# Optimization experiments

Measured on AMD Instinct MI355X. Metric: run time of the kernel, lower is better.

## Reference

```python
import jax, jax.numpy as jnp
import numpy as np
import math

D = 1024
H = 16
EPS = 1e-5

def _layernorm(x, gamma, beta):
    mu = jnp.mean(x, axis=-1, keepdims=True)
    var = jnp.var(x, axis=-1, keepdims=True)
    return (x - mu) * jax.lax.rsqrt(var + EPS) * gamma + beta

def setup_inputs() -> dict:
    key = jax.random.key(0)
    ks = jax.random.split(key, 6)
    B, T = 2, 2048
    x = jax.random.normal(ks[0], (B, T, D), dtype=jnp.float32)
    s = 1.0 / math.sqrt(D)
    Wq = jax.random.normal(ks[1], (D, D), dtype=jnp.float32) * s
    Wk = jax.random.normal(ks[2], (D, D), dtype=jnp.float32) * s
    Wv = jax.random.normal(ks[3], (D, D), dtype=jnp.float32) * s
    gamma = jnp.ones((D,), dtype=jnp.float32)
    beta = jnp.zeros((D,), dtype=jnp.float32)
    return {"x": x, "Wq": Wq, "Wk": Wk, "Wv": Wv, "gamma": gamma, "beta": beta}

def reference(x, Wq, Wk, Wv, gamma, beta):
    B, T, Dm = x.shape
    hd = Dm // H
    xn = _layernorm(x, gamma, beta)
    # torch Linear (no bias): y = x @ W.T
    q = (xn @ Wq.T).reshape(B, T, H, hd)
    k = (xn @ Wk.T).reshape(B, T, H, hd)
    v = (xn @ Wv.T).reshape(B, T, H, hd)
    scale = 1.0 / math.sqrt(hd)
    att = jnp.einsum('bnhd,bmhd->bnmh', q, k) * scale  # B,T,T,H
    w = jax.nn.softmax(att, axis=2)  # softmax over key dim m
    y = jnp.einsum('bnmh,bmhd->bnhd', w, v).reshape(B, T, Dm)
    return x + y
```

## Files before the change

### kernel.cpp

```cpp
#include <hip/hip_runtime.h>
#include <hip/hip_bf16.h>
#include <stdint.h>

#define D_MODEL 1024
#define T_SEQ   2048
#define NB      2
#define NH      16
#define HD      64
#define MTOK    4096

typedef __bf16  bf16x8 __attribute__((ext_vector_type(8)));
typedef float   f32x4  __attribute__((ext_vector_type(4)));
typedef float   f32x16 __attribute__((ext_vector_type(16)));

#define GPTR(p) ((const __attribute__((address_space(1))) void*)(p))
#define LPTR(p) ((__attribute__((address_space(3))) void*)(p))

static __device__ __forceinline__ ushort f2bf(float f) {
    union { float f; uint32_t u; } c{f};
    uint32_t u = c.u;
    return (ushort)((u + 0x7fff + ((u >> 16) & 1)) >> 16);
}

static __device__ __forceinline__ unsigned cvt_pk_bf16(float lo, float hi) {
    unsigned r;
    asm("v_cvt_pk_bf16_f32 %0, %1, %2" : "=v"(r) : "v"(lo), "v"(hi));
    return r;
}

#if defined(__has_builtin)
#if __has_builtin(__builtin_amdgcn_exp2f)
#define FEXP2(x) __builtin_amdgcn_exp2f(x)
#endif
#endif
#ifndef FEXP2
static __device__ __forceinline__ float fexp2_asm(float x) {
    float r;
    asm("v_exp_f32 %0, %1" : "=v"(r) : "v"(x));
    return r;
}
#define FEXP2(x) fexp2_asm(x)
#endif

__global__ __launch_bounds__(256) void prep_kernel(const float* __restrict__ x,
                                                   const float* __restrict__ gamma,
                                                   const float* __restrict__ beta,
                                                   ushort* __restrict__ xn,
                                                   const float* __restrict__ a0,
                                                   const float* __restrict__ a1,
                                                   const float* __restrict__ a2,
                                                   ushort* __restrict__ o0,
                                                   ushort* __restrict__ o1,
                                                   ushort* __restrict__ o2) {
    int blk = blockIdx.x;
    int tid = threadIdx.x;
    if (blk >= MTOK) {
        int z = (blk - MTOK) >> 10;
        int cb = (blk - MTOK) & 1023;
        const float* a = (z == 0) ? a0 : (z == 1) ? a1 : a2;
        ushort* o = (z == 0) ? o0 : (z == 1) ? o1 : o2;
        int i = cb * 256 + tid;
        float4 v = ((const float4*)a)[i];
        ushort4 r;
        r.x = f2bf(v.x); r.y = f2bf(v.y); r.z = f2bf(v.z); r.w = f2bf(v.w);
        ((ushort4*)o)[i] = r;
        return;
    }
    int row = blk;
    const float4* xr = (const float4*)(x + (size_t)row * D_MODEL);
    float4 v = xr[tid];
    float s  = v.x + v.y + v.z + v.w;
    float ss = v.x * v.x + v.y * v.y + v.z * v.z + v.w * v.w;
    #pragma unroll
    for (int m = 1; m < 64; m <<= 1) {
        s  += __shfl_xor(s, m);
        ss += __shfl_xor(ss, m);
    }
    __shared__ float red[8];
    int w = tid >> 6, lane = tid & 63;
    if (lane == 0) { red[w] = s; red[4 + w] = ss; }
    __syncthreads();
    s  = red[0] + red[1] + red[2] + red[3];
    ss = red[4] + red[5] + red[6] + red[7];
    float mu   = s * (1.0f / D_MODEL);
    float var  = ss * (1.0f / D_MODEL) - mu * mu;
    float rstd = rsqrtf(var + 1e-5f);
    float4 g = ((const float4*)gamma)[tid];
    float4 b = ((const float4*)beta)[tid];
    ushort4 o;
    o.x = f2bf((v.x - mu) * rstd * g.x + b.x);
    o.y = f2bf((v.y - mu) * rstd * g.y + b.y);
    o.z = f2bf((v.z - mu) * rstd * g.z + b.z);
    o.w = f2bf((v.w - mu) * rstd * g.w + b.w);
    ((ushort4*)(xn + (size_t)row * D_MODEL))[tid] = o;
}

__global__ __launch_bounds__(256) void gemm_qkv(const ushort* __restrict__ A,
                                                const ushort* __restrict__ w0,
                                                const ushort* __restrict__ w1,
                                                const ushort* __restrict__ w2,
                                                ushort* __restrict__ c0,
                                                ushort* __restrict__ c1,
                                                ushort* __restrict__ c2,
                                                int M, int N, int K) {
    const ushort* Bw = (blockIdx.z == 0) ? w0 : (blockIdx.z == 1) ? w1 : w2;
    ushort* C = (blockIdx.z == 0) ? c0 : (blockIdx.z == 1) ? c1 : c2;

    __shared__ __align__(16) ushort lA[2][128 * 64];
    __shared__ __align__(16) ushort lB[2][128 * 64];
    int tid = threadIdx.x;
    int w = tid >> 6, lane = tid & 63;
    int wr = w >> 1, wc = w & 1;
    int l15 = lane & 15, l4 = lane >> 4;
    int row0 = blockIdx.x * 128, col0 = blockIdx.y * 128;

    f32x4 zero = {0.f, 0.f, 0.f, 0.f};
    f32x4 acc[4][4];
    #pragma unroll
    for (int i = 0; i < 4; ++i)
        #pragma unroll
        for (int j = 0; j < 4; ++j) acc[i][j] = zero;

    int sr  = tid >> 3;
    int scc = (((tid & 7) ^ (sr & 7)) << 3);
    int rch[2];
    rch[0] = ((l4)     ^ (l15 & 7)) << 4;
    rch[1] = ((4 + l4) ^ (l15 & 7)) << 4;

    auto STAGE = [&](int buf, int kt) {
        int k0 = kt * 64;
        #pragma unroll
        for (int i = 0; i < 4; ++i) {
            int r = i * 32 + sr;
            const ushort* ga = A + (size_t)(row0 + r) * K + k0 + scc;
            __builtin_amdgcn_global_load_lds(GPTR(ga), LPTR((char*)lA[buf] + i * 4096 + tid * 16), 16, 0, 0);
            const ushort* gb = Bw + (size_t)(col0 + r) * K + k0 + scc;
            __builtin_amdgcn_global_load_lds(GPTR(gb), LPTR((char*)lB[buf] + i * 4096 + tid * 16), 16, 0, 0);
        }
    };

    STAGE(0, 0);
    __syncthreads();

    int buf = 0;
    const int NK = K / 64;
    for (int kt = 0; kt < NK; ++kt) {
        if (kt + 1 < NK) STAGE(buf ^ 1, kt + 1);
        const char* la  = (const char*)lA[buf];
        const char* lb_ = (const char*)lB[buf];
        __builtin_amdgcn_s_setprio(1);
        #pragma unroll
        for (int ks = 0; ks < 2; ++ks) {
            bf16x8 af[4], bfr[4];
            #pragma unroll
            for (int i = 0; i < 4; ++i) {
                int ra = wr * 64 + i * 16 + l15;
                int rb = wc * 64 + i * 16 + l15;
                af[i]  = *(const bf16x8*)(la  + ra * 128 + rch[ks]);
                bfr[i] = *(const bf16x8*)(lb_ + rb * 128 + rch[ks]);
            }
            #pragma unroll
            for (int i = 0; i < 4; ++i)
                #pragma unroll
                for (int j = 0; j < 4; ++j)
                    acc[i][j] = __builtin_amdgcn_mfma_f32_16x16x32_bf16(af[i], bfr[j], acc[i][j], 0, 0, 0);
        }
        __builtin_amdgcn_s_setprio(0);
        __syncthreads();
        buf ^= 1;
    }

    if (blockIdx.z == 2) {
        #pragma unroll
        for (int i = 0; i < 4; ++i) {
            int rbase = row0 + wr * 64 + i * 16 + l4 * 4;
            #pragma unroll
            for (int j = 0; j < 4; ++j) {
                int col = col0 + wc * 64 + j * 16 + l15;
                ushort4 o4;
                o4.x = f2bf(acc[i][j][0]);
                o4.y = f2bf(acc[i][j][1]);
                o4.z = f2bf(acc[i][j][2]);
                o4.w = f2bf(acc[i][j][3]);
                *(ushort4*)&C[(size_t)col * M + rbase] = o4;
            }
        }
    } else {
        float sc = (blockIdx.z == 0) ? 0.18033688011112042f : 1.0f;
        #pragma unroll
        for (int i = 0; i < 4; ++i) {
            int rbase = row0 + wr * 64 + i * 16 + l4 * 4;
            #pragma unroll
            for (int j = 0; j < 4; ++j) {
                int col = col0 + wc * 64 + j * 16 + l15;
                #pragma unroll
                for (int r = 0; r < 4; ++r)
                    C[(size_t)(rbase + r) * N + col] = f2bf(acc[i][j][r] * sc);
            }
        }
    }
}

__global__ __launch_bounds__(256, 2) void attn_kernel(const ushort* __restrict__ Q,
                                                      const ushort* __restrict__ Km,
                                                      const ushort* __restrict__ Vt,
                                                      const float* __restrict__ x,
                                                      float* __restrict__ out) {
    int bid = blockIdx.x;
    int sw  = (bid & 7) * 64 + (bid >> 3);
    int qt = sw & 15, h = (sw >> 4) & 15, b = sw >> 8;

    int tid = threadIdx.x, w = tid >> 6, lane = tid & 63;
    int l31 = lane & 31, hh = lane >> 5, x7 = lane & 7;
    size_t head_off = (size_t)b * T_SEQ * D_MODEL + (size_t)h * HD;
    const ushort* Qh  = Q  + head_off;
    const ushort* Kh  = Km + head_off;
    const ushort* Vth = Vt + (size_t)h * HD * MTOK + (size_t)b * T_SEQ;

    __shared__ __align__(16) ushort lK[4][64 * 64];
    __shared__ __align__(16) ushort lV[4][64 * 64];

    int qrow = qt * 128 + w * 32 + l31;
    bf16x8 qf[4];
    #pragma unroll
    for (int c = 0; c < 4; ++c)
        qf[c] = *(const bf16x8*)&Qh[(size_t)qrow * D_MODEL + hh * 8 + c * 16];

    int i0  = w * 128 + lane;
    int r0  = i0 >> 3;
    int cg0 = (i0 & 7) ^ (r0 & 7);
    const ushort* ksrc0 = Kh  + (size_t)r0 * D_MODEL + cg0 * 8;
    const ushort* ksrc1 = ksrc0 + (size_t)8 * D_MODEL;
    const ushort* vsrc0 = Vth + (size_t)r0 * MTOK + cg0 * 8;
    const ushort* vsrc1 = vsrc0 + (size_t)8 * MTOK;

    int chv[4];
    #pragma unroll
    for (int c = 0; c < 4; ++c) chv[c] = ((hh + 2 * c) ^ x7) << 4;

    f32x16 oa[2], ob[2], zvec;
    float la = 0.f, lb = 0.f;
    #pragma unroll
    for (int i = 0; i < 16; ++i) {
        oa[0][i] = 0.f; oa[1][i] = 0.f; ob[0][i] = 0.f; ob[1][i] = 0.f;
        zvec[i] = 0.f;
    }

    auto STAGE = [&](int t) {
        size_t kb = (size_t)t * 64;
        char* dk = (char*)lK[t & 3] + w * 2048;
        char* dv = (char*)lV[t & 3] + w * 2048;
        __builtin_amdgcn_global_load_lds(GPTR(ksrc0 + kb * D_MODEL), LPTR(dk), 16, 0, 0);
        __builtin_amdgcn_global_load_lds(GPTR(ksrc1 + kb * D_MODEL), LPTR(dk + 1024), 16, 0, 0);
        __builtin_amdgcn_global_load_lds(GPTR(vsrc0 + kb), LPTR(dv), 16, 0, 0);
        __builtin_amdgcn_global_load_lds(GPTR(vsrc1 + kb), LPTR(dv + 1024), 16, 0, 0);
    };

    auto QK = [&](int t, f32x16& sa, f32x16& sb) {
        const char* lKc = (const char*)lK[t & 3];
        __builtin_amdgcn_s_setprio(1);
        {
            bf16x8 ka  = *(const bf16x8*)(lKc + l31 * 128 + chv[0]);
            bf16x8 kb2 = *(const bf16x8*)(lKc + (32 + l31) * 128 + chv[0]);
            sa = __builtin_amdgcn_mfma_f32_32x32x16_bf16(ka,  qf[0], zvec, 0, 0, 0);
            sb = __builtin_amdgcn_mfma_f32_32x32x16_bf16(kb2, qf[0], zvec, 0, 0, 0);
        }
        #pragma unroll
        for (int c = 1; c < 4; ++c) {
            bf16x8 ka  = *(const bf16x8*)(lKc + l31 * 128 + chv[c]);
            bf16x8 kb2 = *(const bf16x8*)(lKc + (32 + l31) * 128 + chv[c]);
            sa = __builtin_amdgcn_mfma_f32_32x32x16_bf16(ka,  qf[c], sa, 0, 0, 0);
            sb = __builtin_amdgcn_mfma_f32_32x32x16_bf16(kb2, qf[c], sb, 0, 0, 0);
        }
        __builtin_amdgcn_s_setprio(0);
    };

    auto SMPV = [&](int t, const f32x16& sa, const f32x16& sb) {
        const char* lVc = (const char*)lV[t & 3];
        bf16x8 vfr[4][2];
        #pragma unroll
        for (int ks = 0; ks < 4; ++ks)
            #pragma unroll
            for (int dblk = 0; dblk < 2; ++dblk)
                vfr[ks][dblk] = *(const bf16x8*)(lVc + (dblk * 32 + l31) * 128 + chv[ks]);

        bf16x8 pfr[4];
        #pragma unroll
        for (int kbb = 0; kbb < 2; ++kbb) {
            float pr[16];
            #pragma unroll
            for (int r = 0; r < 16; ++r) pr[r] = FEXP2(kbb ? sb[r] : sa[r]);
            float s0 = (pr[0] + pr[1]) + (pr[2] + pr[3]);
            float s1 = (pr[4] + pr[5]) + (pr[6] + pr[7]);
            float s2 = (pr[8] + pr[9]) + (pr[10] + pr[11]);
            float s3 = (pr[12] + pr[13]) + (pr[14] + pr[15]);
            if (kbb == 0) la += (s0 + s1) + (s2 + s3);
            else          lb += (s0 + s1) + (s2 + s3);
            #pragma unroll
            for (int sl = 0; sl < 2; ++sl) {
                unsigned pA = cvt_pk_bf16(pr[sl * 8 + 0], pr[sl * 8 + 1]);
                unsigned pB = cvt_pk_bf16(pr[sl * 8 + 2], pr[sl * 8 + 3]);
                unsigned pC = cvt_pk_bf16(pr[sl * 8 + 4], pr[sl * 8 + 5]);
                unsigned pD = cvt_pk_bf16(pr[sl * 8 + 6], pr[sl * 8 + 7]);
                asm("v_permlane32_swap_b32 %0, %1" : "+v"(pA), "+v"(pC));
                asm("v_permlane32_swap_b32 %0, %1" : "+v"(pB), "+v"(pD));
                union { unsigned u[4]; bf16x8 v; } pf;
                pf.u[0] = pA; pf.u[1] = pB; pf.u[2] = pC; pf.u[3] = pD;
                pfr[kbb * 2 + sl] = pf.v;
            }
        }
        __builtin_amdgcn_s_setprio(1);
        #pragma unroll
        for (int ks = 0; ks < 4; ++ks) {
            #pragma unroll
            for (int dblk = 0; dblk < 2; ++dblk) {
                if (ks & 1)
                    ob[dblk] = __builtin_amdgcn_mfma_f32_32x32x16_bf16(vfr[ks][dblk], pfr[ks], ob[dblk], 0, 0, 0);
                else
                    oa[dblk] = __builtin_amdgcn_mfma_f32_32x32x16_bf16(vfr[ks][dblk], pfr[ks], oa[dblk], 0, 0, 0);
            }
        }
        __builtin_amdgcn_s_setprio(0);
    };

    STAGE(0);
    STAGE(1);
    __syncthreads();

    const int NT = T_SEQ / 64;
    for (int s = 0; s < NT / 2; ++s) {
        int t0 = 2 * s;
        if (s < NT / 2 - 1) { STAGE(t0 + 2); STAGE(t0 + 3); }
        f32x16 sa0, sb0, sa1, sb1;
        QK(t0, sa0, sb0);
        QK(t0 + 1, sa1, sb1);
        SMPV(t0, sa0, sb0);
        SMPV(t0 + 1, sa1, sb1);
        __syncthreads();
    }

    float Lt = la + lb;
    float Lfull = Lt + __shfl_xor(Lt, 32);
    float inv = 1.0f / Lfull;
    const float* xrow = x   + (size_t)(b * T_SEQ + qrow) * D_MODEL + h * HD + 4 * hh;
    float*       orow = out + (size_t)(b * T_SEQ + qrow) * D_MODEL + h * HD + 4 * hh;
    #pragma unroll
    for (int dblk = 0; dblk < 2; ++dblk) {
        #pragma unroll
        for (int g = 0; g < 4; ++g) {
            int coff = dblk * 32 + 8 * g;
            float4 xv = *(const float4*)(xrow + coff);
            float4 ov;
            ov.x = xv.x + (oa[dblk][4 * g + 0] + ob[dblk][4 * g + 0]) * inv;
            ov.y = xv.y + (oa[dblk][4 * g + 1] + ob[dblk][4 * g + 1]) * inv;
            ov.z = xv.z + (oa[dblk][4 * g + 2] + ob[dblk][4 * g + 2]) * inv;
            ov.w = xv.w + (oa[dblk][4 * g + 3] + ob[dblk][4 * g + 3]) * inv;
            *(float4*)(orow + coff) = ov;
        }
    }
}

extern "C" void kernel_launch(void* const* d_in, const int* in_sizes, int n_in,
                              void* d_out, int out_size, void* d_ws, size_t ws_size,
                              hipStream_t stream) {
    const float* x     = (const float*)d_in[0];
    const float* Wq    = (const float*)d_in[1];
    const float* Wk    = (const float*)d_in[2];
    const float* Wv    = (const float*)d_in[3];
    const float* gamma = (const float*)d_in[4];
    const float* beta  = (const float*)d_in[5];
    float* out = (float*)d_out;

    char* ws = (char*)d_ws;
    ushort* xn  = (ushort*)(ws);
    ushort* wqb = (ushort*)(ws + (8  << 20));
    ushort* wkb = (ushort*)(ws + (10 << 20));
    ushort* wvb = (ushort*)(ws + (12 << 20));
    ushort* Qb  = (ushort*)(ws + (14 << 20));
    ushort* Kb  = (ushort*)(ws + (22 << 20));
    ushort* Vtb = (ushort*)(ws + (30 << 20));

    int M = NB * T_SEQ;

    prep_kernel<<<dim3(MTOK + 3072), 256, 0, stream>>>(x, gamma, beta, xn,
                                                       Wq, Wk, Wv, wqb, wkb, wvb);
    gemm_qkv<<<dim3(M / 128, D_MODEL / 128, 3), 256, 0, stream>>>(
        xn, wqb, wkb, wvb, Qb, Kb, Vtb, M, D_MODEL, D_MODEL);
    attn_kernel<<<dim3(512), 256, 0, stream>>>(Qb, Kb, Vtb, x, out);
}
```

Measured before the change: 98.22 us.

## Split attention key range into two partitions and combine partials in a separate kernel

The attention kernel now splits the key sequence into two halves, launching twice as many blocks (1024) with a 2-stage LDS buffer, fewer live registers and launch bounds raised to 4 blocks per CU. This is meant to raise occupancy and fill the GPU better than 512 blocks did. One partition writes fp32 partial outputs into the output buffer, the other writes bf16 partials into workspace, and both write row sums. A new combine kernel adds the two partials, normalizes and adds the residual. The cost is an extra kernel launch, extra memory traffic, and bf16 rounding of one partial sum. The softmax has no max subtraction, so partials combine without rescaling.

```diff
diff --git a/kernel.cpp b/kernel.cpp
--- a/kernel.cpp
+++ b/kernel.cpp
@@ -20,6 +20,11 @@
     union { float f; uint32_t u; } c{f};
     uint32_t u = c.u;
     return (ushort)((u + 0x7fff + ((u >> 16) & 1)) >> 16);
+}
+
+static __device__ __forceinline__ float bf2f(ushort u) {
+    union { uint32_t u; float f; } c{(uint32_t)u << 16};
+    return c.f;
 }
 
 static __device__ __forceinline__ unsigned cvt_pk_bf16(float lo, float hi) {
@@ -201,24 +206,25 @@
     }
 }
 
-__global__ __launch_bounds__(256, 2) void attn_kernel(const ushort* __restrict__ Q,
+__global__ __launch_bounds__(256, 4) void attn_kernel(const ushort* __restrict__ Q,
                                                       const ushort* __restrict__ Km,
                                                       const ushort* __restrict__ Vt,
-                                                      const float* __restrict__ x,
-                                                      float* __restrict__ out) {
+                                                      float* __restrict__ o32,
+                                                      ushort* __restrict__ o16,
+                                                      float* __restrict__ Lp) {
     int bid = blockIdx.x;
-    int sw  = (bid & 7) * 64 + (bid >> 3);
-    int qt = sw & 15, h = (sw >> 4) & 15, b = sw >> 8;
+    int sw  = (bid & 7) * 128 + (bid >> 3);
+    int qt = sw & 15, p = (sw >> 4) & 1, h = (sw >> 5) & 15, b = sw >> 9;
 
     int tid = threadIdx.x, w = tid >> 6, lane = tid & 63;
     int l31 = lane & 31, hh = lane >> 5, x7 = lane & 7;
     size_t head_off = (size_t)b * T_SEQ * D_MODEL + (size_t)h * HD;
     const ushort* Qh  = Q  + head_off;
-    const ushort* Kh  = Km + head_off;
-    const ushort* Vth = Vt + (size_t)h * HD * MTOK + (size_t)b * T_SEQ;
-
-    __shared__ __align__(16) ushort lK[4][64 * 64];
-    __shared__ __align__(16) ushort lV[4][64 * 64];
+    const ushort* Kh  = Km + head_off + (size_t)(p * 1024) * D_MODEL;
+    const ushort* Vth = Vt + (size_t)h * HD * MTOK + (size_t)b * T_SEQ + p * 1024;
+
+    __shared__ __align__(16) ushort lK[2][64 * 64];
+    __shared__ __align__(16) ushort lV[2][64 * 64];
 
     int qrow = qt * 128 + w * 32 + l31;
     bf16x8 qf[4];
@@ -238,64 +244,51 @@
     #pragma unroll
     for (int c = 0; c < 4; ++c) chv[c] = ((hh + 2 * c) ^ x7) << 4;
 
-    f32x16 oa[2], ob[2], zvec;
-    float la = 0.f, lb = 0.f;
+    f32x16 o[2], zvec;
+    float lsum = 0.f;
     #pragma unroll
-    for (int i = 0; i < 16; ++i) {
-        oa[0][i] = 0.f; oa[1][i] = 0.f; ob[0][i] = 0.f; ob[1][i] = 0.f;
-        zvec[i] = 0.f;
-    }
+    for (int i = 0; i < 16; ++i) { o[0][i] = 0.f; o[1][i] = 0.f; zvec[i] = 0.f; }
 
     auto STAGE = [&](int t) {
         size_t kb = (size_t)t * 64;
-        char* dk = (char*)lK[t & 3] + w * 2048;
-        char* dv = (char*)lV[t & 3] + w * 2048;
+        char* dk = (char*)lK[t & 1] + w * 2048;
+        char* dv = (char*)lV[t & 1] + w * 2048;
         __builtin_amdgcn_global_load_lds(GPTR(ksrc0 + kb * D_MODEL), LPTR(dk), 16, 0, 0);
         __builtin_amdgcn_global_load_lds(GPTR(ksrc1 + kb * D_MODEL), LPTR(dk + 1024), 16, 0, 0);
         __builtin_amdgcn_global_load_lds(GPTR(vsrc0 + kb), LPTR(dv), 16, 0, 0);
         __builtin_amdgcn_global_load_lds(GPTR(vsrc1 + kb), LPTR(dv + 1024), 16, 0, 0);
     };
 
-    auto QK = [&](int t, f32x16& sa, f32x16& sb) {
-        const char* lKc = (const char*)lK[t & 3];
-        __builtin_amdgcn_s_setprio(1);
-        {
-            bf16x8 ka  = *(const bf16x8*)(lKc + l31 * 128 + chv[0]);
-            bf16x8 kb2 = *(const bf16x8*)(lKc + (32 + l31) * 128 + chv[0]);
-            sa = __builtin_amdgcn_mfma_f32_32x32x16_bf16(ka,  qf[0], zvec, 0, 0, 0);
-            sb = __builtin_amdgcn_mfma_f32_32x32x16_bf16(kb2, qf[0], zvec, 0, 0, 0);
-        }
-        #pragma unroll
-        for (int c = 1; c < 4; ++c) {
-            bf16x8 ka  = *(const bf16x8*)(lKc + l31 * 128 + chv[c]);
-            bf16x8 kb2 = *(const bf16x8*)(lKc + (32 + l31) * 128 + chv[c]);
-            sa = __builtin_amdgcn_mfma_f32_32x32x16_bf16(ka,  qf[c], sa, 0, 0, 0);
-            sb = __builtin_amdgcn_mfma_f32_32x32x16_bf16(kb2, qf[c], sb, 0, 0, 0);
-        }
-        __builtin_amdgcn_s_setprio(0);
-    };
-
-    auto SMPV = [&](int t, const f32x16& sa, const f32x16& sb) {
-        const char* lVc = (const char*)lV[t & 3];
-        bf16x8 vfr[4][2];
-        #pragma unroll
-        for (int ks = 0; ks < 4; ++ks)
-            #pragma unroll
-            for (int dblk = 0; dblk < 2; ++dblk)
-                vfr[ks][dblk] = *(const bf16x8*)(lVc + (dblk * 32 + l31) * 128 + chv[ks]);
-
-        bf16x8 pfr[4];
-        #pragma unroll
-        for (int kbb = 0; kbb < 2; ++kbb) {
+    STAGE(0);
+    __syncthreads();
+
+    for (int t = 0; t < 16; ++t) {
+        if (t < 15) STAGE(t + 1);
+        const char* lKc = (const char*)lK[t & 1];
+        const char* lVc = (const char*)lV[t & 1];
+        #pragma unroll
+        for (int half = 0; half < 2; ++half) {
+            f32x16 s;
+            __builtin_amdgcn_s_setprio(1);
+            {
+                bf16x8 kf = *(const bf16x8*)(lKc + (half * 32 + l31) * 128 + chv[0]);
+                s = __builtin_amdgcn_mfma_f32_32x32x16_bf16(kf, qf[0], zvec, 0, 0, 0);
+            }
+            #pragma unroll
+            for (int c = 1; c < 4; ++c) {
+                bf16x8 kf = *(const bf16x8*)(lKc + (half * 32 + l31) * 128 + chv[c]);
+                s = __builtin_amdgcn_mfma_f32_32x32x16_bf16(kf, qf[c], s, 0, 0, 0);
+            }
+            __builtin_amdgcn_s_setprio(0);
             float pr[16];
             #pragma unroll
-            for (int r = 0; r < 16; ++r) pr[r] = FEXP2(kbb ? sb[r] : sa[r]);
+            for (int r = 0; r < 16; ++r) pr[r] = FEXP2(s[r]);
             float s0 = (pr[0] + pr[1]) + (pr[2] + pr[3]);
             float s1 = (pr[4] + pr[5]) + (pr[6] + pr[7]);
             float s2 = (pr[8] + pr[9]) + (pr[10] + pr[11]);
             float s3 = (pr[12] + pr[13]) + (pr[14] + pr[15]);
-            if (kbb == 0) la += (s0 + s1) + (s2 + s3);
-            else          lb += (s0 + s1) + (s2 + s3);
+            lsum += (s0 + s1) + (s2 + s3);
+            bf16x8 pfr[2];
             #pragma unroll
             for (int sl = 0; sl < 2; ++sl) {
                 unsigned pA = cvt_pk_bf16(pr[sl * 8 + 0], pr[sl * 8 + 1]);
@@ -306,58 +299,73 @@
                 asm("v_permlane32_swap_b32 %0, %1" : "+v"(pB), "+v"(pD));
                 union { unsigned u[4]; bf16x8 v; } pf;
                 pf.u[0] = pA; pf.u[1] = pB; pf.u[2] = pC; pf.u[3] = pD;
-                pfr[kbb * 2 + sl] = pf.v;
-            }
+                pfr[sl] = pf.v;
+            }
+            __builtin_amdgcn_s_setprio(1);
+            #pragma unroll
+            for (int sl = 0; sl < 2; ++sl) {
+                int ks = half * 2 + sl;
+                #pragma unroll
+                for (int dblk = 0; dblk < 2; ++dblk) {
+                    bf16x8 vf = *(const bf16x8*)(lVc + (dblk * 32 + l31) * 128 + chv[ks]);
+                    o[dblk] = __builtin_amdgcn_mfma_f32_32x32x16_bf16(vf, pfr[sl], o[dblk], 0, 0, 0);
+                }
+            }
+            __builtin_amdgcn_s_setprio(0);
         }
-        __builtin_amdgcn_s_setprio(1);
-        #pragma unroll
-        for (int ks = 0; ks < 4; ++ks) {
-            #pragma unroll
-            for (int dblk = 0; dblk < 2; ++dblk) {
-                if (ks & 1)
-                    ob[dblk] = __builtin_amdgcn_mfma_f32_32x32x16_bf16(vfr[ks][dblk], pfr[ks], ob[dblk], 0, 0, 0);
-                else
-                    oa[dblk] = __builtin_amdgcn_mfma_f32_32x32x16_bf16(vfr[ks][dblk], pfr[ks], oa[dblk], 0, 0, 0);
-            }
-        }
-        __builtin_amdgcn_s_setprio(0);
-    };
-
-    STAGE(0);
-    STAGE(1);
-    __syncthreads();
-
-    const int NT = T_SEQ / 64;
-    for (int s = 0; s < NT / 2; ++s) {
-        int t0 = 2 * s;
-        if (s < NT / 2 - 1) { STAGE(t0 + 2); STAGE(t0 + 3); }
-        f32x16 sa0, sb0, sa1, sb1;
-        QK(t0, sa0, sb0);
-        QK(t0 + 1, sa1, sb1);
-        SMPV(t0, sa0, sb0);
-        SMPV(t0 + 1, sa1, sb1);
         __syncthreads();
     }
 
-    float Lt = la + lb;
-    float Lfull = Lt + __shfl_xor(Lt, 32);
-    float inv = 1.0f / Lfull;
-    const float* xrow = x   + (size_t)(b * T_SEQ + qrow) * D_MODEL + h * HD + 4 * hh;
-    float*       orow = out + (size_t)(b * T_SEQ + qrow) * D_MODEL + h * HD + 4 * hh;
-    #pragma unroll
-    for (int dblk = 0; dblk < 2; ++dblk) {
-        #pragma unroll
-        for (int g = 0; g < 4; ++g) {
-            int coff = dblk * 32 + 8 * g;
-            float4 xv = *(const float4*)(xrow + coff);
-            float4 ov;
-            ov.x = xv.x + (oa[dblk][4 * g + 0] + ob[dblk][4 * g + 0]) * inv;
-            ov.y = xv.y + (oa[dblk][4 * g + 1] + ob[dblk][4 * g + 1]) * inv;
-            ov.z = xv.z + (oa[dblk][4 * g + 2] + ob[dblk][4 * g + 2]) * inv;
-            ov.w = xv.w + (oa[dblk][4 * g + 3] + ob[dblk][4 * g + 3]) * inv;
-            *(float4*)(orow + coff) = ov;
-        }
-    }
+    float Lt = lsum + __shfl_xor(lsum, 32);
+    size_t tok = (size_t)(b * T_SEQ) + qrow;
+    if (hh == 0) Lp[(size_t)p * (MTOK * NH) + tok * NH + h] = Lt;
+    size_t ebase = tok * D_MODEL + h * HD + 4 * hh;
+    if (p == 0) {
+        #pragma unroll
+        for (int dblk = 0; dblk < 2; ++dblk)
+            #pragma unroll
+            for (int g = 0; g < 4; ++g) {
+                float4 ov;
+                ov.x = o[dblk][4 * g + 0];
+                ov.y = o[dblk][4 * g + 1];
+                ov.z = o[dblk][4 * g + 2];
+                ov.w = o[dblk][4 * g + 3];
+                *(float4*)(o32 + ebase + dblk * 32 + 8 * g) = ov;
+            }
+    } else {
+        #pragma unroll
+        for (int dblk = 0; dblk < 2; ++dblk)
+            #pragma unroll
+            for (int g = 0; g < 4; ++g) {
+                ushort4 ov;
+                ov.x = f2bf(o[dblk][4 * g + 0]);
+                ov.y = f2bf(o[dblk][4 * g + 1]);
+                ov.z = f2bf(o[dblk][4 * g + 2]);
+                ov.w = f2bf(o[dblk][4 * g + 3]);
+                *(ushort4*)(o16 + ebase + dblk * 32 + 8 * g) = ov;
+            }
+    }
+}
+
+__global__ __launch_bounds__(256) void combine_kernel(const float* __restrict__ x,
+                                                      const ushort* __restrict__ o16,
+                                                      const float* __restrict__ Lp,
+                                                      float* __restrict__ out) {
+    int i = blockIdx.x * 256 + threadIdx.x;
+    int tok = i >> 8;
+    int h = (i >> 4) & 15;
+    size_t li = (size_t)tok * NH + h;
+    float l = Lp[li] + Lp[(size_t)(MTOK * NH) + li];
+    float inv = 1.0f / l;
+    float4 o0 = ((const float4*)out)[i];
+    ushort4 u = ((const ushort4*)o16)[i];
+    float4 xv = ((const float4*)x)[i];
+    float4 r;
+    r.x = xv.x + (o0.x + bf2f(u.x)) * inv;
+    r.y = xv.y + (o0.y + bf2f(u.y)) * inv;
+    r.z = xv.z + (o0.z + bf2f(u.z)) * inv;
+    r.w = xv.w + (o0.w + bf2f(u.w)) * inv;
+    ((float4*)out)[i] = r;
 }
 
 extern "C" void kernel_launch(void* const* d_in, const int* in_sizes, int n_in,
@@ -380,11 +388,15 @@
     ushort* Kb  = (ushort*)(ws + (22 << 20));
     ushort* Vtb = (ushort*)(ws + (30 << 20));
 
+    ushort* o16 = (ushort*)(ws);
+    float*  Lp  = (float*)(ws + (8 << 20));
+
     int M = NB * T_SEQ;
 
     prep_kernel<<<dim3(MTOK + 3072), 256, 0, stream>>>(x, gamma, beta, xn,
                                                        Wq, Wk, Wv, wqb, wkb, wvb);
     gemm_qkv<<<dim3(M / 128, D_MODEL / 128, 3), 256, 0, stream>>>(
         xn, wqb, wkb, wvb, Qb, Kb, Vtb, M, D_MODEL, D_MODEL);
-    attn_kernel<<<dim3(512), 256, 0, stream>>>(Qb, Kb, Vtb, x, out);
-}
+    attn_kernel<<<dim3(1024), 256, 0, stream>>>(Qb, Kb, Vtb, out, o16, Lp);
+    combine_kernel<<<dim3(4096), 256, 0, stream>>>(x, o16, Lp, out);
+}
```

New measurement: 107.4 us. 9.4% more time.
